# Performance work log

Measured on AMD Instinct MI355X. Metric: run time of the kernel, lower is better.

Reference implementation:

```python
import jax, jax.numpy as jnp
import numpy as np

NQ, NL, E = 100000, 16384, 1000000
C_IN, C_OUT, D = 128, 4, 3
H = 64        # kernel MLP hidden
PH = 256      # projection hidden


def setup_inputs() -> dict:
    key = jax.random.key(0)
    ks = jax.random.split(key, 16)
    s = 0.05
    return {
        "rndata_flat": jax.random.normal(ks[0], (NL, C_IN), jnp.float32),
        "phys_pos_query": jax.random.uniform(ks[1], (NQ, D), jnp.float32),
        "latent_tokens_pos": jax.random.uniform(ks[2], (NL, D), jnp.float32),
        "edge_index_dst": jax.random.randint(ks[3], (E,), 0, NQ),
        "edge_index_src": jax.random.randint(ks[4], (E,), 0, NL),
        # kernel MLP: (2*D) -> 64 -> 64 -> C_IN, gelu between layers
        "W0": jax.random.normal(ks[5], (2 * D, H), jnp.float32) * s,
        "b0": jnp.zeros((H,), jnp.float32),
        "W1": jax.random.normal(ks[6], (H, H), jnp.float32) * s,
        "b1": jnp.zeros((H,), jnp.float32),
        "W2": jax.random.normal(ks[7], (H, C_IN), jnp.float32) * s,
        "b2": jnp.zeros((C_IN,), jnp.float32),
        # projection ChannelMLP: C_IN -> 256 -> C_OUT, gelu between layers
        "P0": jax.random.normal(ks[8], (C_IN, PH), jnp.float32) * s,
        "pb0": jnp.zeros((PH,), jnp.float32),
        "P1": jax.random.normal(ks[9], (PH, C_OUT), jnp.float32) * s,
        "pb1": jnp.zeros((C_OUT,), jnp.float32),
    }


def reference(rndata_flat, phys_pos_query, latent_tokens_pos,
              edge_index_dst, edge_index_src,
              W0, b0, W1, b1, W2, b2, P0, pb0, P1, pb1):
    nq = phys_pos_query.shape[0]
    # --- IntegralTransform, transform_type='linear', single scale ---
    # gather edge endpoint coordinates: [E, 2*D]
    e_in = jnp.concatenate(
        [phys_pos_query[edge_index_dst], latent_tokens_pos[edge_index_src]], axis=-1)
    # kernel MLP per edge
    h = jax.nn.gelu(e_in @ W0 + b0)
    h = jax.nn.gelu(h @ W1 + b1)
    k = h @ W2 + b2                                   # [E, C_IN]
    # linear transform: kernel * gathered source features
    rep = k * rndata_flat[edge_index_src]             # [E, C_IN]
    # mean aggregation (scatter) over query nodes
    sums = jax.ops.segment_sum(rep, edge_index_dst, num_segments=nq)
    cnt = jax.ops.segment_sum(jnp.ones((rep.shape[0], 1), rep.dtype),
                              edge_index_dst, num_segments=nq)
    agg = sums / jnp.maximum(cnt, 1.0)                # [Nq, C_IN]
    # --- projection ChannelMLP (2 layers) ---
    h2 = jax.nn.gelu(agg @ P0 + pb0)
    return h2 @ P1 + pb1                              # [Nq, C_OUT]
```

## Files before the change

### kernel.cpp

```cpp
#include <hip/hip_runtime.h>


#define BLOCK 256

typedef _Float16 half8 __attribute__((ext_vector_type(8)));
typedef float f32x4 __attribute__((ext_vector_type(4)));


__device__ __forceinline__ float gelu_f(float x) {
    float x3 = x * x * x;
    float t  = 0.7978845608028654f * fmaf(0.044715f, x3, x);
    float e  = __expf(2.0f * t);
    float r  = __builtin_amdgcn_rcpf(e + 1.0f);
    return 0.5f * x * (1.0f + (1.0f - 2.0f * r));
}


__global__ void hist_kernel(const int* __restrict__ dst, int* __restrict__ hist, int E) {
    int e = blockIdx.x * blockDim.x + threadIdx.x;
    if (e < E) atomicAdd(&hist[dst[e]], 1);
}

__global__ __launch_bounds__(1024) void scan_kernel(const int* __restrict__ hist,
                                                    int* __restrict__ start, int n) {
    __shared__ int wsum[16];
    __shared__ int woff[16];
    int tid = threadIdx.x;
    int lane = tid & 63, wid = tid >> 6;
    int carry = 0;
    for (int base = 0; base < n; base += 1024) {
        int i = base + tid;
        int v = (i < n) ? hist[i] : 0;
        int incl = v;
#pragma unroll
        for (int off = 1; off < 64; off <<= 1) {
            int t = __shfl_up(incl, off, 64);
            if (lane >= off) incl += t;
        }
        if (lane == 63) wsum[wid] = incl;
        __syncthreads();
        if (tid == 0) {
            int acc = carry;
#pragma unroll
            for (int w = 0; w < 16; ++w) { woff[w] = acc; acc += wsum[w]; }
            carry = acc;
        }
        __syncthreads();
        if (i < n) start[i] = woff[wid] + incl - v;
        __syncthreads();
    }
    if (threadIdx.x == 0) start[n] = carry;
}

__global__ void scatter_kernel(const int* __restrict__ dst, const int* __restrict__ src,
                               const int* __restrict__ start, int* __restrict__ cursor,
                               int* __restrict__ dsts, int* __restrict__ srcs, int E) {
    int e = blockIdx.x * blockDim.x + threadIdx.x;
    if (e >= E) return;
    int d = dst[e];
    int pos = start[d] + atomicAdd(&cursor[d], 1);
    dsts[pos] = d;
    srcs[pos] = src[e];
}


__global__ void wprep_kernel(const float* __restrict__ W1,
                             const float* __restrict__ W2,
                             char* __restrict__ img) {
    union { _Float16 h[8]; uint4 u; } cv;
    for (int task = threadIdx.x; task < 1536; task += 256) {
        bool isW2 = task >= 512;
        int id = isW2 ? task - 512 : task;
        int n = id >> 3, kc = id & 7;
        const float* W = isW2 ? W2 : W1;
        int N = isW2 ? 128 : 64;
#pragma unroll
        for (int j = 0; j < 8; ++j) cv.h[j] = (_Float16)W[(kc * 8 + j) * N + n];
        *(uint4*)(img + (isW2 ? 8192 : 0) + n * 128 + ((kc ^ (n & 7)) * 16)) = cv.u;
    }
}


template <int QB, bool FUSED_PROJ>
__global__ __launch_bounds__(BLOCK, 2) void fused_kernel(
    const float* __restrict__ rndata,
    const float* __restrict__ qpos,
    const float* __restrict__ lpos,
    const int*   __restrict__ dsts,
    const int*   __restrict__ srcs,
    const int*   __restrict__ start,
    const float* __restrict__ W0, const float* __restrict__ b0,
    const float* __restrict__ b1, const float* __restrict__ b2,
    const uint4* __restrict__ wimg,
    const float* __restrict__ P0, const float* __restrict__ pb0,
    const float* __restrict__ P1, const float* __restrict__ pb1,
    float* __restrict__ agg,
    float* __restrict__ out,
    int nq)
{
    extern __shared__ char smemc[];
    float* sacc = (float*)(smemc + 32768);
    const int tid = threadIdx.x;

    {
        uint4* wdst = (uint4*)smemc;
        for (int i = tid; i < 1536; i += BLOCK) wdst[i] = wimg[i];
    }
    for (int i = tid; i < QB * 129; i += BLOCK) sacc[i] = 0.f;

    const int q0   = blockIdx.x * QB;
    const int qend = min(q0 + QB, nq);
    const int e0 = start[q0], e1 = start[qend];
    const int ntl = (e1 - e0 + 15) >> 4;

    const int m   = tid & 63;
    const int wid = tid >> 6;
    const int c16 = m & 15;
    const int g   = m >> 4;

    char* hb = smemc + 24576 + wid * 2048;
    const int aoff0 = c16 * 128 + (((0 + g) ^ (c16 & 7)) * 16);
    const int aoff1 = c16 * 128 + (((4 + g) ^ (c16 & 7)) * 16);

    float b1v[4], b2v[8];
#pragma unroll
    for (int nt = 0; nt < 4; ++nt) b1v[nt] = b1[nt * 16 + c16];
#pragma unroll
    for (int nt = 0; nt < 8; ++nt) b2v[nt] = b2[nt * 16 + c16];

    __syncthreads();

    for (int t = wid; t < ntl; t += 4) {
        const int eb = e0 + (t << 4);

        const int  eA = eb + c16;
        const bool vA = eA < e1;
        const int  dA = vA ? dsts[eA] : q0;
        const int  sA = vA ? srcs[eA] : 0;

        int s_ep[4], soff[4];
        bool v_ep[4];
#pragma unroll
        for (int i = 0; i < 4; ++i) {
            int ee = eb + g * 4 + i;
            v_ep[i] = ee < e1;
            int d   = v_ep[i] ? dsts[ee] : q0;
            s_ep[i] = v_ep[i] ? srcs[ee] : 0;
            soff[i] = (d - q0) * 129 + c16;
        }

        float pin[6];
        {
            const float* pq = qpos + dA * 3;
            pin[0] = pq[0]; pin[1] = pq[1]; pin[2] = pq[2];
            const float* pl = lpos + sA * 3;
            pin[3] = pl[0]; pin[4] = pl[1]; pin[5] = pl[2];
        }

        float C0[16];
        {
            const float* b0p = b0 + g * 8;
            *(float4*)&C0[0]  = *(const float4*)(b0p);
            *(float4*)&C0[4]  = *(const float4*)(b0p + 4);
            *(float4*)&C0[8]  = *(const float4*)(b0p + 32);
            *(float4*)&C0[12] = *(const float4*)(b0p + 36);
        }
#pragma unroll
        for (int k = 0; k < 6; ++k) {
            const float a  = pin[k];
            const float* w = W0 + k * 64 + g * 8;
            float wv[16];
            *(float4*)&wv[0]  = *(const float4*)(w);
            *(float4*)&wv[4]  = *(const float4*)(w + 4);
            *(float4*)&wv[8]  = *(const float4*)(w + 32);
            *(float4*)&wv[12] = *(const float4*)(w + 36);
#pragma unroll
            for (int j = 0; j < 16; ++j) C0[j] = fmaf(a, wv[j], C0[j]);
        }
        union { _Float16 h[8]; half8 v; } u0, u1;
#pragma unroll
        for (int j = 0; j < 8; ++j) u0.h[j] = (_Float16)gelu_f(C0[j]);
#pragma unroll
        for (int j = 0; j < 8; ++j) u1.h[j] = (_Float16)gelu_f(C0[8 + j]);
        const half8 a0 = u0.v, a1 = u1.v;

#pragma unroll
        for (int nt = 0; nt < 4; ++nt) {
            const int  nrow = nt * 16 + c16;
            const char* wb  = smemc + nrow * 128;
            half8 bb0 = *(const half8*)(wb + (((0 + g) ^ (nrow & 7)) * 16));
            half8 bb1 = *(const half8*)(wb + (((4 + g) ^ (nrow & 7)) * 16));
            f32x4 acc = {b1v[nt], b1v[nt], b1v[nt], b1v[nt]};
            acc = __builtin_amdgcn_mfma_f32_16x16x32_f16(a0, bb0, acc, 0, 0, 0);
            acc = __builtin_amdgcn_mfma_f32_16x16x32_f16(a1, bb1, acc, 0, 0, 0);
#pragma unroll
            for (int i = 0; i < 4; ++i) {
                const int row  = g * 4 + i;
                const int colh = nt * 16 + c16;
                *(_Float16*)(hb + row * 128 + (((colh >> 3) ^ (row & 7)) * 16)
                             + (colh & 7) * 2) = (_Float16)gelu_f(acc[i]);
            }
        }
        const half8 a2 = *(const half8*)(hb + aoff0);
        const half8 a3 = *(const half8*)(hb + aoff1);

        f32x4 rAv, rBv;
#pragma unroll
        for (int i = 0; i < 4; ++i)
            rAv[i] = rndata[(size_t)s_ep[i] * 128 + c16];
#pragma unroll
        for (int nt = 0; nt < 8; ++nt) {
            if (nt < 7) {
                if (nt & 1) {
#pragma unroll
                    for (int i = 0; i < 4; ++i)
                        rAv[i] = rndata[(size_t)s_ep[i] * 128 + (nt + 1) * 16 + c16];
                } else {
#pragma unroll
                    for (int i = 0; i < 4; ++i)
                        rBv[i] = rndata[(size_t)s_ep[i] * 128 + (nt + 1) * 16 + c16];
                }
            }
            const int  nrow = nt * 16 + c16;
            const char* wb  = smemc + 8192 + nrow * 128;
            half8 bb0 = *(const half8*)(wb + (((0 + g) ^ (nrow & 7)) * 16));
            half8 bb1 = *(const half8*)(wb + (((4 + g) ^ (nrow & 7)) * 16));
            f32x4 acc = {b2v[nt], b2v[nt], b2v[nt], b2v[nt]};
            acc = __builtin_amdgcn_mfma_f32_16x16x32_f16(a2, bb0, acc, 0, 0, 0);
            acc = __builtin_amdgcn_mfma_f32_16x16x32_f16(a3, bb1, acc, 0, 0, 0);
#pragma unroll
            for (int i = 0; i < 4; ++i) {
                float rc = (nt & 1) ? rBv[i] : rAv[i];
                if (v_ep[i]) atomicAdd(&sacc[soff[i] + nt * 16], acc[i] * rc);
            }
        }
    }
    __syncthreads();

    if (!FUSED_PROJ) {
        for (int idx = tid; idx < QB * 128; idx += BLOCK) {
            int ql = idx >> 7, c = idx & 127;
            int q  = q0 + ql;
            if (q < qend) {
                float deg = (float)(start[q + 1] - start[q]);
                agg[(size_t)q * 128 + c] = sacc[ql * 129 + c] / fmaxf(deg, 1.f);
            }
        }
    } else {
        if (tid < QB) {
            int q = q0 + tid;
            if (q < nq) {
                float deg = (float)(start[q + 1] - start[q]);
                float inv = 1.0f / fmaxf(deg, 1.f);
                const float* aq = &sacc[tid * 129];
                float o0 = pb1[0], o1 = pb1[1], o2 = pb1[2], o3 = pb1[3];
#pragma unroll 1
                for (int jj = 0; jj < 256; jj += 8) {
                    float acc[8];
#pragma unroll
                    for (int u = 0; u < 8; ++u) acc[u] = pb0[jj + u];
#pragma unroll
                    for (int i = 0; i < 128; ++i) {
                        float av = aq[i] * inv;
#pragma unroll
                        for (int u = 0; u < 8; ++u)
                            acc[u] = fmaf(av, P0[i * 256 + jj + u], acc[u]);
                    }
#pragma unroll
                    for (int u = 0; u < 8; ++u) {
                        float h = gelu_f(acc[u]);
                        o0 = fmaf(h, P1[(jj + u) * 4 + 0], o0);
                        o1 = fmaf(h, P1[(jj + u) * 4 + 1], o1);
                        o2 = fmaf(h, P1[(jj + u) * 4 + 2], o2);
                        o3 = fmaf(h, P1[(jj + u) * 4 + 3], o3);
                    }
                }
                float4* o4 = (float4*)(out + (size_t)q * 4);
                *o4 = make_float4(o0, o1, o2, o3);
            }
        }
    }
}


__global__ __launch_bounds__(256) void proj_kernel(
    const float* __restrict__ agg,
    const float* __restrict__ P0, const float* __restrict__ pb0,
    const float* __restrict__ P1, const float* __restrict__ pb1,
    float* __restrict__ out, int nq)
{
    int q = blockIdx.x * blockDim.x + threadIdx.x;
    if (q >= nq) return;

    float a[128];
    const float4* ag4 = (const float4*)(agg + (size_t)q * 128);
#pragma unroll
    for (int i = 0; i < 32; ++i) {
        float4 v = ag4[i];
        a[4 * i + 0] = v.x; a[4 * i + 1] = v.y;
        a[4 * i + 2] = v.z; a[4 * i + 3] = v.w;
    }

    float o0 = pb1[0], o1 = pb1[1], o2 = pb1[2], o3 = pb1[3];
#pragma unroll 1
    for (int jj = 0; jj < 256; jj += 8) {
        float acc[8];
#pragma unroll
        for (int u = 0; u < 8; ++u) acc[u] = pb0[jj + u];
#pragma unroll
        for (int i = 0; i < 128; ++i) {
            float av = a[i];
#pragma unroll
            for (int u = 0; u < 8; ++u)
                acc[u] = fmaf(av, P0[i * 256 + jj + u], acc[u]);
        }
#pragma unroll
        for (int u = 0; u < 8; ++u) {
            float h = gelu_f(acc[u]);
            o0 = fmaf(h, P1[(jj + u) * 4 + 0], o0);
            o1 = fmaf(h, P1[(jj + u) * 4 + 1], o1);
            o2 = fmaf(h, P1[(jj + u) * 4 + 2], o2);
            o3 = fmaf(h, P1[(jj + u) * 4 + 3], o3);
        }
    }
    float4* o4 = (float4*)(out + (size_t)q * 4);
    *o4 = make_float4(o0, o1, o2, o3);
}

extern "C" void kernel_launch(void* const* d_in, const int* in_sizes, int n_in,
                              void* d_out, int out_size, void* d_ws, size_t ws_size,
                              hipStream_t stream)
{
    const float* rndata = (const float*)d_in[0];
    const float* qpos   = (const float*)d_in[1];
    const float* lpos   = (const float*)d_in[2];
    const int*   dst    = (const int*)d_in[3];
    const int*   src    = (const int*)d_in[4];
    const float* W0  = (const float*)d_in[5];
    const float* b0  = (const float*)d_in[6];
    const float* W1  = (const float*)d_in[7];
    const float* b1  = (const float*)d_in[8];
    const float* W2  = (const float*)d_in[9];
    const float* b2  = (const float*)d_in[10];
    const float* P0  = (const float*)d_in[11];
    const float* pb0 = (const float*)d_in[12];
    const float* P1  = (const float*)d_in[13];
    const float* pb1 = (const float*)d_in[14];

    int nq = in_sizes[1] / 3;
    int E  = in_sizes[3];

    size_t agg_bytes  = (size_t)nq * 128 * sizeof(float);
    size_t sort_bytes = 0;
    {
        size_t o = 0;
        o += ((size_t)nq * sizeof(int) + 15) & ~(size_t)15;
        o += ((size_t)nq * sizeof(int) + 15) & ~(size_t)15;
        o += ((size_t)(nq + 1) * sizeof(int) + 15) & ~(size_t)15;
        o += ((size_t)E * sizeof(int) + 15) & ~(size_t)15;
        o += ((size_t)E * sizeof(int) + 15) & ~(size_t)15;
        o += 24576;
        sort_bytes = o;
    }
    bool path_a = (agg_bytes + sort_bytes) <= ws_size;

    size_t off = path_a ? agg_bytes : 0;
    auto alloc = [&](size_t bytes) {
        void* p = (char*)d_ws + off;
        off += (bytes + 15) & ~(size_t)15;
        return p;
    };
    float* agg   = (float*)d_ws;
    int* hist    = (int*)alloc((size_t)nq * sizeof(int));
    int* cursor  = (int*)alloc((size_t)nq * sizeof(int));
    int* start   = (int*)alloc((size_t)(nq + 1) * sizeof(int));
    int* dsts    = (int*)alloc((size_t)E * sizeof(int));
    int* srcs    = (int*)alloc((size_t)E * sizeof(int));
    uint4* wimg  = (uint4*)alloc(24576);

    size_t histpad = ((size_t)nq * sizeof(int) + 15) & ~(size_t)15;
    hipMemsetAsync(hist, 0, 2 * histpad, stream);

    wprep_kernel<<<1, 256, 0, stream>>>(W1, W2, (char*)wimg);
    hist_kernel<<<(E + 255) / 256, 256, 0, stream>>>(dst, hist, E);
    scan_kernel<<<1, 1024, 0, stream>>>(hist, start, nq);
    scatter_kernel<<<(E + 255) / 256, 256, 0, stream>>>(dst, src, start, cursor, dsts, srcs, E);

    constexpr int    QB   = 12;
    constexpr size_t SMEM = 32768 + (size_t)QB * 129 * 4;
    int nb = (nq + QB - 1) / QB;

    if (path_a) {
        fused_kernel<QB, false><<<nb, BLOCK, SMEM, stream>>>(
            rndata, qpos, lpos, dsts, srcs, start,
            W0, b0, b1, b2, wimg, P0, pb0, P1, pb1, agg, nullptr, nq);
        proj_kernel<<<(nq + 255) / 256, 256, 0, stream>>>(
            agg, P0, pb0, P1, pb1, (float*)d_out, nq);
    } else {
        fused_kernel<QB, true><<<nb, BLOCK, SMEM, stream>>>(
            rndata, qpos, lpos, dsts, srcs, start,
            W0, b0, b1, b2, wimg, P0, pb0, P1, pb1, nullptr, (float*)d_out, nq);
    }
}
```

Baseline: 1.187 ms.

## Read MFMA weight fragments directly from global memory instead of staging in LDS

The W1/W2 fp16 weight image is re-laid out per MFMA fragment, so each lane loads its B operand with one contiguous 16-byte global read, which should be served from L1/L2 cache. The per-block copy of 24 KB of weights into shared memory is removed, which cuts LDS from about 38 KB to about 14 KB per block and drops the block prologue. The cost is that every tile iteration now issues global/cache loads for the weights instead of LDS reads, which adds latency on the inner MFMA loop.

```diff
diff --git a/kernel.cpp b/kernel.cpp
--- a/kernel.cpp
+++ b/kernel.cpp
@@ -66,17 +66,19 @@
 
 __global__ void wprep_kernel(const float* __restrict__ W1,
                              const float* __restrict__ W2,
-                             char* __restrict__ img) {
+                             uint4* __restrict__ img) {
     union { _Float16 h[8]; uint4 u; } cv;
     for (int task = threadIdx.x; task < 1536; task += 256) {
         bool isW2 = task >= 512;
         int id = isW2 ? task - 512 : task;
-        int n = id >> 3, kc = id & 7;
+        int n = id >> 3, ks = id & 7;
         const float* W = isW2 ? W2 : W1;
         int N = isW2 ? 128 : 64;
 #pragma unroll
-        for (int j = 0; j < 8; ++j) cv.h[j] = (_Float16)W[(kc * 8 + j) * N + n];
-        *(uint4*)(img + (isW2 ? 8192 : 0) + n * 128 + ((kc ^ (n & 7)) * 16)) = cv.u;
+        for (int j = 0; j < 8; ++j) cv.h[j] = (_Float16)W[(ks * 8 + j) * N + n];
+        int nt = n >> 4, c16 = n & 15, g = ks & 3, hi = ks >> 2;
+        int unit = (isW2 ? 512 : 0) + ((nt * 2 + hi) * 16 + c16) * 4 + g;
+        img[unit] = cv.u;
     }
 }
 
@@ -99,13 +101,9 @@
     int nq)
 {
     extern __shared__ char smemc[];
-    float* sacc = (float*)(smemc + 32768);
+    float* sacc = (float*)(smemc + 8192);
     const int tid = threadIdx.x;
 
-    {
-        uint4* wdst = (uint4*)smemc;
-        for (int i = tid; i < 1536; i += BLOCK) wdst[i] = wimg[i];
-    }
     for (int i = tid; i < QB * 129; i += BLOCK) sacc[i] = 0.f;
 
     const int q0   = blockIdx.x * QB;
@@ -118,9 +116,11 @@
     const int c16 = m & 15;
     const int g   = m >> 4;
 
-    char* hb = smemc + 24576 + wid * 2048;
+    char* hb = smemc + wid * 2048;
     const int aoff0 = c16 * 128 + (((0 + g) ^ (c16 & 7)) * 16);
     const int aoff1 = c16 * 128 + (((4 + g) ^ (c16 & 7)) * 16);
+
+    const char* wimgc = (const char*)wimg + c16 * 64 + g * 16;
 
     float b1v[4], b2v[8];
 #pragma unroll
@@ -186,10 +186,8 @@
 
 #pragma unroll
         for (int nt = 0; nt < 4; ++nt) {
-            const int  nrow = nt * 16 + c16;
-            const char* wb  = smemc + nrow * 128;
-            half8 bb0 = *(const half8*)(wb + (((0 + g) ^ (nrow & 7)) * 16));
-            half8 bb1 = *(const half8*)(wb + (((4 + g) ^ (nrow & 7)) * 16));
+            half8 bb0 = *(const half8*)(wimgc + nt * 2048);
+            half8 bb1 = *(const half8*)(wimgc + nt * 2048 + 1024);
             f32x4 acc = {b1v[nt], b1v[nt], b1v[nt], b1v[nt]};
             acc = __builtin_amdgcn_mfma_f32_16x16x32_f16(a0, bb0, acc, 0, 0, 0);
             acc = __builtin_amdgcn_mfma_f32_16x16x32_f16(a1, bb1, acc, 0, 0, 0);
@@ -221,10 +219,8 @@
                         rBv[i] = rndata[(size_t)s_ep[i] * 128 + (nt + 1) * 16 + c16];
                 }
             }
-            const int  nrow = nt * 16 + c16;
-            const char* wb  = smemc + 8192 + nrow * 128;
-            half8 bb0 = *(const half8*)(wb + (((0 + g) ^ (nrow & 7)) * 16));
-            half8 bb1 = *(const half8*)(wb + (((4 + g) ^ (nrow & 7)) * 16));
+            half8 bb0 = *(const half8*)(wimgc + 8192 + nt * 2048);
+            half8 bb1 = *(const half8*)(wimgc + 8192 + nt * 2048 + 1024);
             f32x4 acc = {b2v[nt], b2v[nt], b2v[nt], b2v[nt]};
             acc = __builtin_amdgcn_mfma_f32_16x16x32_f16(a2, bb0, acc, 0, 0, 0);
             acc = __builtin_amdgcn_mfma_f32_16x16x32_f16(a3, bb1, acc, 0, 0, 0);
@@ -381,13 +377,13 @@
     size_t histpad = ((size_t)nq * sizeof(int) + 15) & ~(size_t)15;
     hipMemsetAsync(hist, 0, 2 * histpad, stream);
 
-    wprep_kernel<<<1, 256, 0, stream>>>(W1, W2, (char*)wimg);
+    wprep_kernel<<<1, 256, 0, stream>>>(W1, W2, wimg);
     hist_kernel<<<(E + 255) / 256, 256, 0, stream>>>(dst, hist, E);
     scan_kernel<<<1, 1024, 0, stream>>>(hist, start, nq);
     scatter_kernel<<<(E + 255) / 256, 256, 0, stream>>>(dst, src, start, cursor, dsts, srcs, E);
 
     constexpr int    QB   = 12;
-    constexpr size_t SMEM = 32768 + (size_t)QB * 129 * 4;
+    constexpr size_t SMEM = 8192 + (size_t)QB * 129 * 4;
     int nb = (nq + QB - 1) / QB;
 
     if (path_a) {
```

After: 1.379 ms. +16.1%, slower.
